# Performance work log

Measured on AMD Instinct MI355X. Metric: run time of the kernel, lower is better.

Reference implementation:

```python
import jax, jax.numpy as jnp
import numpy as np

B, T, D, F, H = 512, 48, 128, 16, 512


def setup_inputs() -> dict:
    key = jax.random.key(0)
    ks = jax.random.split(key, 7)
    return {
        "input": jax.random.normal(ks[0], (B, T, D, F), dtype=jnp.float32),
        "attn_w": jax.random.normal(ks[1], (2 * H + F * T,), dtype=jnp.float32) * 0.02,
        "attn_b": jax.random.normal(ks[2], (1,), dtype=jnp.float32) * 0.02,
        "w_ih": jax.random.normal(ks[3], (4 * H, D * F), dtype=jnp.float32) * 0.02,
        "w_hh": jax.random.normal(ks[4], (4 * H, H), dtype=jnp.float32) * 0.02,
        "b_ih": jax.random.normal(ks[5], (4 * H,), dtype=jnp.float32) * 0.02,
        "b_hh": jax.random.normal(ks[6], (4 * H,), dtype=jnp.float32) * 0.02,
    }


def reference(input, attn_w, attn_b, w_ih, w_hh, b_ih, b_hh):
    Bsz, Ts, Dn, Fn = input.shape
    Hs = w_hh.shape[1]
    # permute(0,2,3,1): [B, T, D, F] -> [B, D, F, T]
    x_perm = jnp.transpose(input, (0, 2, 3, 1))
    x_flat = x_perm.reshape(Bsz, Dn, Fn * Ts)  # [B, D, F*T]
    # encode_attn input is concat(hidden, cell, x); split the weight accordingly
    w_h, w_c, w_x = attn_w[:Hs], attn_w[Hs:2 * Hs], attn_w[2 * Hs:]
    # x contribution to attention logits is constant across steps
    e_x = x_flat @ w_x + attn_b[0]             # [B, D]
    xs = jnp.moveaxis(x_perm, 3, 0)            # [T, B, D, F] (time-major for scan)
    bias = b_ih + b_hh                         # fuse the two LSTM biases

    def step(carry, x_t):
        h, c = carry                           # [B, H] each
        e = e_x + (h @ w_h)[:, None] + (c @ w_c)[:, None]  # [B, D]
        a = jax.nn.softmax(e, axis=-1)
        x_hat = (a[:, :, None] * x_t).reshape(Bsz, Dn * Fn)  # [B, D*F]
        gates = x_hat @ w_ih.T + h @ w_hh.T + bias            # [B, 4H]
        i, f, g, o = jnp.split(gates, 4, axis=-1)  # torch LSTM gate order
        c_new = jax.nn.sigmoid(f) * c + jax.nn.sigmoid(i) * jnp.tanh(g)
        h_new = jax.nn.sigmoid(o) * jnp.tanh(c_new)
        return (h_new, c_new), h_new

    h0 = jnp.zeros((Bsz, Hs), dtype=input.dtype)
    _, hs = jax.lax.scan(step, (h0, h0), xs)   # hs: [T, B, H]
    return jnp.transpose(hs, (1, 0, 2))        # [B, T, H] == hidden_states[:, 1:]
```

## Files before the change

kernel.cpp:

```cpp
#include <hip/hip_runtime.h>

#define B_ 512
#define T_ 48
#define D_ 128
#define F_ 16
#define H_ 512

typedef float f32x4 __attribute__((ext_vector_type(4)));
typedef short s16x8 __attribute__((ext_vector_type(8)));
typedef unsigned short u16x8 __attribute__((ext_vector_type(8)));
typedef unsigned short u16x4 __attribute__((ext_vector_type(4)));
typedef unsigned long long u64;

__device__ __forceinline__ unsigned short f2bf(float x) {
  unsigned u = __float_as_uint(x);
  u += 0x7fffu + ((u >> 16) & 1u);
  return (unsigned short)(u >> 16);
}
__device__ __forceinline__ float bf2f(unsigned short h) {
  return __uint_as_float(((unsigned)h) << 16);
}
__device__ __forceinline__ float fsig(float x) {
  float e = __builtin_amdgcn_exp2f(-1.442695041f * x);
  return __builtin_amdgcn_rcpf(1.f + e);
}
__device__ __forceinline__ float ftanh(float x) {
  float e = __builtin_amdgcn_exp2f(2.885390082f * x);
  return 1.f - 2.f * __builtin_amdgcn_rcpf(1.f + e);
}

__device__ __forceinline__ void st_sys_u64(u64* p, u64 v) {
  __hip_atomic_store(p, v, __ATOMIC_RELAXED, __HIP_MEMORY_SCOPE_SYSTEM);
}
__device__ __forceinline__ u64 ld_sys_u64(const u64* p) {
  return __hip_atomic_load((u64*)p, __ATOMIC_RELAXED, __HIP_MEMORY_SCOPE_SYSTEM);
}
__device__ __forceinline__ void st_sys_u16(unsigned short* p, unsigned short v) {
  __hip_atomic_store(p, v, __ATOMIC_RELAXED, __HIP_MEMORY_SCOPE_SYSTEM);
}
__device__ __forceinline__ void st_sys_u32(unsigned* p, unsigned v) {
  __hip_atomic_store(p, v, __ATOMIC_RELAXED, __HIP_MEMORY_SCOPE_SYSTEM);
}
__device__ __forceinline__ unsigned ld_sys_u32(const unsigned* p) {
  return __hip_atomic_load((unsigned*)p, __ATOMIC_RELAXED, __HIP_MEMORY_SCOPE_SYSTEM);
}

#define AS1 __attribute__((address_space(1)))
#define AS3 __attribute__((address_space(3)))
__device__ __forceinline__ void g2lds16(const void* g, void* l) {
  __builtin_amdgcn_global_load_lds((const AS1 void*)g, (AS3 void*)l, 16, 0, 0);
}

__global__ __launch_bounds__(256) void k_prep(const float* __restrict__ wih,
                                              const float* __restrict__ whh,
                                              unsigned short* __restrict__ wih_b,
                                              unsigned short* __restrict__ whh_b) {
  long i4 = ((long)blockIdx.x * 256 + threadIdx.x) * 4;
  if (i4 < 4194304) {
    float4 v = *(const float4*)(wih + i4);
    u16x4 o = {f2bf(v.x), f2bf(v.y), f2bf(v.z), f2bf(v.w)};
    *(u16x4*)(wih_b + i4) = o;
  } else {
    long j = i4 - 4194304;
    if (j < 1048576) {
      float4 v = *(const float4*)(whh + j);
      u16x4 o = {f2bf(v.x), f2bf(v.y), f2bf(v.z), f2bf(v.w)};
      *(u16x4*)(whh_b + j) = o;
    }
  }
}

__global__ __launch_bounds__(128) void k_ex(const float* __restrict__ in,
                                            const float* __restrict__ attn_w,
                                            const float* __restrict__ attn_b,
                                            float* __restrict__ a_out) {
  __shared__ float wx[768];
  __shared__ float red[128];
  const int b = blockIdx.x, d = threadIdx.x;
  for (int i = d; i < 768; i += 128) wx[i] = attn_w[1024 + i];
  __syncthreads();
  const float* base = in + (long)b * 98304 + (long)d * 16;
  float acc = 0.f;
  for (int t = 0; t < 48; ++t) {
    const float4* p = (const float4*)(base + (long)t * 2048);
    float4 v0 = p[0], v1 = p[1], v2 = p[2], v3 = p[3];
    acc += v0.x * wx[t]       + v0.y * wx[48 + t]  + v0.z * wx[96 + t]  + v0.w * wx[144 + t];
    acc += v1.x * wx[192 + t] + v1.y * wx[240 + t] + v1.z * wx[288 + t] + v1.w * wx[336 + t];
    acc += v2.x * wx[384 + t] + v2.y * wx[432 + t] + v2.z * wx[480 + t] + v2.w * wx[528 + t];
    acc += v3.x * wx[576 + t] + v3.y * wx[624 + t] + v3.z * wx[672 + t] + v3.w * wx[720 + t];
  }
  acc += attn_b[0];
  red[d] = acc;
  __syncthreads();
  for (int s = 64; s > 0; s >>= 1) {
    if (d < s) red[d] = fmaxf(red[d], red[d + s]);
    __syncthreads();
  }
  float mx = red[0];
  __syncthreads();
  float ex = expf(acc - mx);
  red[d] = ex;
  __syncthreads();
  for (int s = 64; s > 0; s >>= 1) {
    if (d < s) red[d] += red[d + s];
    __syncthreads();
  }
  a_out[b * 128 + d] = ex / red[0];
}

__global__ __launch_bounds__(256) void k_xhat(const float* __restrict__ in,
                                              const float* __restrict__ a,
                                              unsigned short* __restrict__ xh) {
  const int mrow = blockIdx.x;
  const int t = mrow >> 9, b = mrow & 511;
  const int tid = threadIdx.x;
  const int k = tid * 8;
  const int d = k >> 4;
  const int f0 = k & 15;
  const float* src = in + (((long)(b * 48 + t) * 128 + d) * 16 + f0);
  float4 v0 = *(const float4*)src;
  float4 v1 = *(const float4*)(src + 4);
  float s = a[b * 128 + d];
  u16x8 o;
  o[0] = f2bf(v0.x * s); o[1] = f2bf(v0.y * s); o[2] = f2bf(v0.z * s); o[3] = f2bf(v0.w * s);
  o[4] = f2bf(v1.x * s); o[5] = f2bf(v1.y * s); o[6] = f2bf(v1.z * s); o[7] = f2bf(v1.w * s);
  *(u16x8*)(xh + (long)mrow * 2048 + k) = o;
}

#define G_STAGEA(ktv, s)                                                        \
  do {                                                                          \
    const long ko_ = (long)(ktv) * 64 + (long)(s) * 262144;                     \
    char* la_ = (char*)SM + ((ktv) & 1) * 32768 + (s) * 16384 + ldsw;           \
    g2lds16(Ag + ko_, la_);                                                     \
    g2lds16(Ag + ko_ + 131072, la_ + 8192);                                     \
  } while (0)

#define G_LDA4(dst, bufel, ksv, mh)                                             \
  do {                                                                          \
    const unsigned short* ab_ =                                                 \
        SM + (bufel) + aBase + (mh) * 4096 + (psw ^ ((ksv) * 32));              \
    dst[0] = *(const s16x8*)(ab_);                                              \
    dst[1] = *(const s16x8*)(ab_ + 1024);                                       \
    dst[2] = *(const s16x8*)(ab_ + 2048);                                       \
    dst[3] = *(const s16x8*)(ab_ + 3072);                                       \
  } while (0)

#define G_LDBG(dst, ktv)                                                        \
  do {                                                                          \
    const unsigned short* bp_ = Bg + (long)(ktv) * 64;                          \
    _Pragma("unroll") for (int nt_ = 0; nt_ < 4; ++nt_)                         \
        _Pragma("unroll") for (int ks_ = 0; ks_ < 2; ++ks_)                     \
            dst[nt_][ks_] = *(const s16x8*)(bp_ + nt_ * 16 * 2048 + ks_ * 32);  \
  } while (0)

#define G_MMA2(mh, Af, BC, ksv)                                                 \
  do {                                                                          \
    __builtin_amdgcn_s_setprio(1);                                              \
    _Pragma("unroll") for (int mt_ = 0; mt_ < 4; ++mt_)                         \
        _Pragma("unroll") for (int nt_ = 0; nt_ < 4; ++nt_)                     \
            acc[(mh) * 4 + mt_][nt_] = __builtin_amdgcn_mfma_f32_16x16x32_bf16( \
                Af[mt_], BC[nt_][ksv], acc[(mh) * 4 + mt_][nt_], 0, 0, 0);      \
    __builtin_amdgcn_s_setprio(0);                                              \
  } while (0)

#define G_GATE(n) asm volatile("s_waitcnt vmcnt(" #n ")" ::: "memory")

#define G_TILE(ktv, BC, BN)                                                     \
  do {                                                                          \
    const int bufel_ = ((ktv) & 1) * 16384;                                     \
    s16x8 a0[4], a1[4];                                                         \
    G_LDBG(BN, (ktv) + 1);                                                      \
    G_LDA4(a0, bufel_, 0, 0);                                                   \
    G_STAGEA((ktv) + 1, 0);                                                     \
    G_STAGEA((ktv) + 1, 1);                                                     \
    G_MMA2(0, a0, BC, 0);                                                       \
    G_LDA4(a1, bufel_, 0, 1);                                                   \
    G_MMA2(1, a1, BC, 0);                                                       \
    G_LDA4(a0, bufel_, 1, 0);                                                   \
    G_MMA2(0, a0, BC, 1);                                                       \
    G_LDA4(a1, bufel_, 1, 1);                                                   \
    G_MMA2(1, a1, BC, 1);                                                       \
    G_GATE(0);                                                                  \
    __builtin_amdgcn_s_barrier();                                               \
  } while (0)

__global__ __launch_bounds__(512, 2) void k_gemm(const unsigned short* __restrict__ A,
                                                 const unsigned short* __restrict__ Bw,
                                                 unsigned short* __restrict__ C) {
  __shared__ __align__(16) unsigned short SM[32768];
  const int tid = threadIdx.x;
  const int w = tid >> 6, lane = tid & 63;
  const int q = lane >> 4, l16 = lane & 15;
  const int wm = w >> 2, wn = w & 3;
  const int id = blockIdx.x;
  const int xcd = id & 7, j = id >> 3;
  const long m0 = ((long)xcd * 12 + (j >> 3)) * 256;
  const long n0 = (long)(j & 7) * 256;

  const int srow = w * 8 + (lane >> 3);
  const int csrc = (lane & 7) ^ (lane >> 3);
  const unsigned short* Ag = A + (m0 + srow) * 2048 + csrc * 8;
  const int ldsw = w * 1024;

  const unsigned short* Bg = Bw + (n0 + wn * 64 + l16) * 2048 + q * 8;

  const int psw = (q ^ (l16 & 7)) * 8;
  const int aBase = (wm * 128 + l16) * 64;

  f32x4 acc[8][4];
  const f32x4 zz = {0.f, 0.f, 0.f, 0.f};
#pragma unroll
  for (int i = 0; i < 8; ++i)
#pragma unroll
    for (int j2 = 0; j2 < 4; ++j2) acc[i][j2] = zz;

  s16x8 bA[4][2], bB[4][2];
  G_LDBG(bA, 0);
  G_STAGEA(0, 0);
  G_STAGEA(0, 1);
  G_GATE(0);
  __builtin_amdgcn_s_barrier();

#pragma unroll 1
  for (int kt2 = 0; kt2 < 15; ++kt2) {
    const int kt = kt2 * 2;
    G_TILE(kt, bA, bB);
    G_TILE(kt + 1, bB, bA);
  }
  G_TILE(30, bA, bB);
  {
    s16x8 a0[4], a1[4];
    G_LDA4(a0, 16384, 0, 0);
    G_MMA2(0, a0, bB, 0);
    G_LDA4(a1, 16384, 0, 1);
    G_MMA2(1, a1, bB, 0);
    G_LDA4(a0, 16384, 1, 0);
    G_MMA2(0, a0, bB, 1);
    G_LDA4(a1, 16384, 1, 1);
    G_MMA2(1, a1, bB, 1);
  }

#pragma unroll
  for (int mh = 0; mh < 2; ++mh)
#pragma unroll
    for (int mt = 0; mt < 4; ++mt)
#pragma unroll
      for (int nt = 0; nt < 4; ++nt)
#pragma unroll
        for (int r = 0; r < 4; ++r) {
          long m = m0 + wm * 128 + mh * 64 + mt * 16 + q * 4 + r;
          long n = n0 + wn * 64 + nt * 16 + l16;
          C[m * 2048 + n] = f2bf(acc[mh * 4 + mt][nt][r]);
        }
}

__global__ __launch_bounds__(256, 1) void k_rec(const unsigned short* __restrict__ gx,
                                                const unsigned short* __restrict__ whh_b,
                                                const float* __restrict__ b_ih,
                                                const float* __restrict__ b_hh,
                                                unsigned short* __restrict__ h_buf,
                                                float* __restrict__ out,
                                                unsigned int* __restrict__ bar) {
  __shared__ __align__(16) float slab[16 * 32 * 36];
  __shared__ __align__(16) unsigned short hs_own[32 * 40];
  const int tid = threadIdx.x;
  const int w = tid >> 6, lane = tid & 63;
  const int q = lane >> 4, l16 = lane & 15;
  const int bt = blockIdx.x & 15, g = blockIdx.x >> 4;
  const int b0 = bt * 32;
  const int pj = tid & 31;
  const int pr0 = (tid >> 5) * 4;
  unsigned int* slots = &bar[bt * 16];
  const int ownw = ((g >> 2) == w);
  const int ownc = g & 3;

  s16x8 wreg[32];
#pragma unroll
  for (int quad = 0; quad < 4; ++quad)
#pragma unroll
    for (int nt = 0; nt < 2; ++nt)
#pragma unroll
      for (int ci = 0; ci < 4; ++ci) {
        const unsigned short* wp =
            whh_b + (long)(quad * 512 + g * 32 + nt * 16 + l16) * 512 + (w * 4 + ci) * 32 + q * 8;
        asm volatile("global_load_dwordx4 %0, %1, off"
                     : "=v"(wreg[(quad * 2 + nt) * 4 + ci]) : "v"(wp) : "memory");
      }
  asm volatile("s_waitcnt vmcnt(0)" ::: "memory");
  __builtin_amdgcn_sched_barrier(0);

  float bias_[4];
#pragma unroll
  for (int qq = 0; qq < 4; ++qq) {
    int jj = qq * 512 + g * 32 + pj;
    bias_[qq] = b_ih[jj] + b_hh[jj];
  }
  float creg[4] = {0.f, 0.f, 0.f, 0.f};
  const f32x4 zz = {0.f, 0.f, 0.f, 0.f};

#define LD_CHUNK(slot, ci)                                                      \
  do {                                                                          \
    long o_ = hbase + (w * 4 + (ci)) * 8;                                       \
    L[slot][0] = ld_sys_u64(hb + o_);                                           \
    L[slot][1] = ld_sys_u64(hb + o_ + 1);                                       \
    L[slot][2] = ld_sys_u64(hb + o_ + 2048);                                    \
    L[slot][3] = ld_sys_u64(hb + o_ + 2049);                                    \
  } while (0)

  for (int t = 0; t < 48; ++t) {
    unsigned short gxr[4][4];
    const unsigned short* gp = gx + ((long)t * 512 + b0 + pr0) * 2048 + g * 32 + pj;
#pragma unroll
    for (int rr = 0; rr < 4; ++rr)
#pragma unroll
      for (int qq = 0; qq < 4; ++qq)
        gxr[qq][rr] = gp[rr * 2048 + qq * 512];

    if (t > 0) {
      const int need = (lane < 4) && !(ownw && lane == ownc);
      const unsigned* fp = &slots[w * 4 + (lane & 3)];
      while (1) {
        unsigned v = need ? ld_sys_u32(fp) : 0xffffffffu;
        if (__all((int)(v >= (unsigned)t))) break;
      }
      u64 L[2][4];
      const u64* hb = (const u64*)(h_buf + ((t - 1) & 1) * (512 * 512));
      const long hbase = (long)(b0 + l16) * 128 + q * 2;
      f32x4 acc[4][2][2];
#pragma unroll
      for (int a = 0; a < 4; ++a)
#pragma unroll
        for (int b = 0; b < 2; ++b)
#pragma unroll
          for (int c = 0; c < 2; ++c) acc[a][b][c] = zz;
      if (!(ownw && 0 == ownc)) LD_CHUNK(0, 0);
#pragma unroll
      for (int ci = 0; ci < 4; ++ci) {
        if (ci < 3 && !(ownw && (ci + 1) == ownc)) LD_CHUNK((ci + 1) & 1, ci + 1);
        s16x8 af0, af1;
        if (ownw && ci == ownc) {
          af0 = *(const s16x8*)&hs_own[l16 * 40 + q * 8];
          af1 = *(const s16x8*)&hs_own[(16 + l16) * 40 + q * 8];
        } else {
          union { u64 u[2]; s16x8 v; } c0, c1;
          c0.u[0] = L[ci & 1][0]; c0.u[1] = L[ci & 1][1];
          c1.u[0] = L[ci & 1][2]; c1.u[1] = L[ci & 1][3];
          af0 = c0.v; af1 = c1.v;
        }
#pragma unroll
        for (int quad = 0; quad < 4; ++quad)
#pragma unroll
          for (int nt = 0; nt < 2; ++nt) {
            acc[quad][nt][0] = __builtin_amdgcn_mfma_f32_16x16x32_bf16(
                af0, wreg[(quad * 2 + nt) * 4 + ci], acc[quad][nt][0], 0, 0, 0);
            acc[quad][nt][1] = __builtin_amdgcn_mfma_f32_16x16x32_bf16(
                af1, wreg[(quad * 2 + nt) * 4 + ci], acc[quad][nt][1], 0, 0, 0);
          }
      }
#pragma unroll
      for (int quad = 0; quad < 4; ++quad)
#pragma unroll
        for (int nt = 0; nt < 2; ++nt)
#pragma unroll
          for (int mh = 0; mh < 2; ++mh)
            *(f32x4*)&slab[((w * 4 + quad) * 32 + nt * 16 + l16) * 36 + mh * 16 + q * 4] =
                acc[quad][nt][mh];
    }
    __syncthreads();

    float hval[4];
    {
      f32x4 gs[4];
      if (t > 0) {
#pragma unroll
        for (int qq = 0; qq < 4; ++qq) {
          f32x4 s0 = *(const f32x4*)&slab[((0 * 4 + qq) * 32 + pj) * 36 + pr0];
          f32x4 s1 = *(const f32x4*)&slab[((1 * 4 + qq) * 32 + pj) * 36 + pr0];
          f32x4 s2 = *(const f32x4*)&slab[((2 * 4 + qq) * 32 + pj) * 36 + pr0];
          f32x4 s3 = *(const f32x4*)&slab[((3 * 4 + qq) * 32 + pj) * 36 + pr0];
          gs[qq] = (s0 + s1) + (s2 + s3);
        }
      } else {
#pragma unroll
        for (int qq = 0; qq < 4; ++qq) gs[qq] = zz;
      }
#pragma unroll
      for (int rr = 0; rr < 4; ++rr) {
        float g0 = gs[0][rr] + bias_[0] + bf2f(gxr[0][rr]);
        float g1 = gs[1][rr] + bias_[1] + bf2f(gxr[1][rr]);
        float g2 = gs[2][rr] + bias_[2] + bf2f(gxr[2][rr]);
        float g3 = gs[3][rr] + bias_[3] + bf2f(gxr[3][rr]);
        float is = fsig(g0);
        float fs = fsig(g1);
        float gt = ftanh(g2);
        float os = fsig(g3);
        creg[rr] = fs * creg[rr] + is * gt;
        hval[rr] = os * ftanh(creg[rr]);
      }
    }
#pragma unroll
    for (int rr = 0; rr < 4; ++rr) {
      unsigned short hb16 = f2bf(hval[rr]);
      hs_own[(pr0 + rr) * 40 + pj] = hb16;
      st_sys_u16(&h_buf[(t & 1) * (512 * 512) + (b0 + pr0 + rr) * 512 + g * 32 + pj], hb16);
    }
    __syncthreads();
    if (t < 47 && tid == 0)
      st_sys_u32(&slots[g], (unsigned)(t + 1));
#pragma unroll
    for (int rr = 0; rr < 4; ++rr)
      __builtin_nontemporal_store(
          hval[rr], &out[(long)(b0 + pr0 + rr) * (T_ * H_) + (long)t * H_ + g * 32 + pj]);
  }
#undef LD_CHUNK
}

extern "C" void kernel_launch(void* const* d_in, const int* in_sizes, int n_in,
                              void* d_out, int out_size, void* d_ws, size_t ws_size,
                              hipStream_t stream) {
  const float* input  = (const float*)d_in[0];
  const float* attn_w = (const float*)d_in[1];
  const float* attn_b = (const float*)d_in[2];
  const float* w_ih   = (const float*)d_in[3];
  const float* w_hh   = (const float*)d_in[4];
  const float* b_ih   = (const float*)d_in[5];
  const float* b_hh   = (const float*)d_in[6];
  float* out = (float*)d_out;

  char* ws = (char*)d_ws;
  unsigned int* bar     = (unsigned int*)ws;
  float* a_ws           = (float*)(ws + 1024);
  unsigned short* h_buf = (unsigned short*)(ws + 263168);
  unsigned short* whh_b = (unsigned short*)(ws + 1311744);
  unsigned short* wih_b = (unsigned short*)(ws + 3408896);
  unsigned short* x_hat = (unsigned short*)(ws + 11797504);
  unsigned short* gxws  = (unsigned short*)(ws + 112460800);

  (void)hipMemsetAsync(d_ws, 0, 1024, stream);
  hipLaunchKernelGGL(k_prep, dim3(5120), dim3(256), 0, stream, w_ih, w_hh, wih_b, whh_b);
  hipLaunchKernelGGL(k_ex, dim3(512), dim3(128), 0, stream, input, attn_w, attn_b, a_ws);
  hipLaunchKernelGGL(k_xhat, dim3(24576), dim3(256), 0, stream, input, a_ws, x_hat);
  hipLaunchKernelGGL(k_gemm, dim3(768), dim3(512), 0, stream, x_hat, wih_b, gxws);
  hipLaunchKernelGGL(k_rec, dim3(256), dim3(256), 0, stream, gxws, whh_b, b_ih, b_hh, h_buf, out, bar);
}
```

Baseline: 852.1 us.

## Stage GEMM B tiles through LDS and split k_ex time loop across two halves

```diff
diff --git a/kernel.cpp b/kernel.cpp
--- a/kernel.cpp
+++ b/kernel.cpp
@@ -70,18 +70,20 @@
   }
 }
 
-__global__ __launch_bounds__(128) void k_ex(const float* __restrict__ in,
+__global__ __launch_bounds__(256) void k_ex(const float* __restrict__ in,
                                             const float* __restrict__ attn_w,
                                             const float* __restrict__ attn_b,
                                             float* __restrict__ a_out) {
   __shared__ float wx[768];
+  __shared__ float red2[256];
   __shared__ float red[128];
-  const int b = blockIdx.x, d = threadIdx.x;
-  for (int i = d; i < 768; i += 128) wx[i] = attn_w[1024 + i];
+  const int b = blockIdx.x, tid = threadIdx.x;
+  const int d = tid & 127, half = tid >> 7;
+  for (int i = tid; i < 768; i += 256) wx[i] = attn_w[1024 + i];
   __syncthreads();
   const float* base = in + (long)b * 98304 + (long)d * 16;
   float acc = 0.f;
-  for (int t = 0; t < 48; ++t) {
+  for (int t = half * 24; t < half * 24 + 24; ++t) {
     const float4* p = (const float4*)(base + (long)t * 2048);
     float4 v0 = p[0], v1 = p[1], v2 = p[2], v3 = p[3];
     acc += v0.x * wx[t]       + v0.y * wx[48 + t]  + v0.z * wx[96 + t]  + v0.w * wx[144 + t];
@@ -89,23 +91,31 @@
     acc += v2.x * wx[384 + t] + v2.y * wx[432 + t] + v2.z * wx[480 + t] + v2.w * wx[528 + t];
     acc += v3.x * wx[576 + t] + v3.y * wx[624 + t] + v3.z * wx[672 + t] + v3.w * wx[720 + t];
   }
-  acc += attn_b[0];
-  red[d] = acc;
+  red2[tid] = acc;
+  __syncthreads();
+  float a2 = 0.f;
+  if (tid < 128) {
+    a2 = red2[tid] + red2[tid + 128] + attn_b[0];
+    red[tid] = a2;
+  }
   __syncthreads();
   for (int s = 64; s > 0; s >>= 1) {
-    if (d < s) red[d] = fmaxf(red[d], red[d + s]);
+    if (tid < s) red[tid] = fmaxf(red[tid], red[tid + s]);
     __syncthreads();
   }
   float mx = red[0];
   __syncthreads();
-  float ex = expf(acc - mx);
-  red[d] = ex;
+  float ex = 0.f;
+  if (tid < 128) {
+    ex = expf(a2 - mx);
+    red[tid] = ex;
+  }
   __syncthreads();
   for (int s = 64; s > 0; s >>= 1) {
-    if (d < s) red[d] += red[d + s];
+    if (tid < s) red[tid] += red[tid + s];
     __syncthreads();
   }
-  a_out[b * 128 + d] = ex / red[0];
+  if (tid < 128) a_out[b * 128 + d] = ex / red[0];
 }
 
 __global__ __launch_bounds__(256) void k_xhat(const float* __restrict__ in,
@@ -127,12 +137,15 @@
   *(u16x8*)(xh + (long)mrow * 2048 + k) = o;
 }
 
-#define G_STAGEA(ktv, s)                                                        \
+
+#define G_STAGE(ktv, s)                                                         \
   do {                                                                          \
     const long ko_ = (long)(ktv) * 64 + (long)(s) * 262144;                     \
     char* la_ = (char*)SM + ((ktv) & 1) * 32768 + (s) * 16384 + ldsw;           \
     g2lds16(Ag + ko_, la_);                                                     \
     g2lds16(Ag + ko_ + 131072, la_ + 8192);                                     \
+    g2lds16(Bg + ko_, la_ + 65536);                                             \
+    g2lds16(Bg + ko_ + 131072, la_ + 73728);                                    \
   } while (0)
 
 #define G_LDA4(dst, bufel, ksv, mh)                                             \
@@ -145,49 +158,31 @@
     dst[3] = *(const s16x8*)(ab_ + 3072);                                       \
   } while (0)
 
-#define G_LDBG(dst, ktv)                                                        \
+#define G_LDB4(dst, bufel, ksv)                                                 \
   do {                                                                          \
-    const unsigned short* bp_ = Bg + (long)(ktv) * 64;                          \
-    _Pragma("unroll") for (int nt_ = 0; nt_ < 4; ++nt_)                         \
-        _Pragma("unroll") for (int ks_ = 0; ks_ < 2; ++ks_)                     \
-            dst[nt_][ks_] = *(const s16x8*)(bp_ + nt_ * 16 * 2048 + ks_ * 32);  \
+    const unsigned short* bb_ = SM + (bufel) + bBase + (psw ^ ((ksv) * 32));    \
+    dst[0] = *(const s16x8*)(bb_);                                              \
+    dst[1] = *(const s16x8*)(bb_ + 1024);                                       \
+    dst[2] = *(const s16x8*)(bb_ + 2048);                                       \
+    dst[3] = *(const s16x8*)(bb_ + 3072);                                       \
   } while (0)
 
-#define G_MMA2(mh, Af, BC, ksv)                                                 \
+#define G_MMA2(mh, Af, Bf)                                                      \
   do {                                                                          \
     __builtin_amdgcn_s_setprio(1);                                              \
     _Pragma("unroll") for (int mt_ = 0; mt_ < 4; ++mt_)                         \
         _Pragma("unroll") for (int nt_ = 0; nt_ < 4; ++nt_)                     \
             acc[(mh) * 4 + mt_][nt_] = __builtin_amdgcn_mfma_f32_16x16x32_bf16( \
-                Af[mt_], BC[nt_][ksv], acc[(mh) * 4 + mt_][nt_], 0, 0, 0);      \
+                Af[mt_], Bf[nt_], acc[(mh) * 4 + mt_][nt_], 0, 0, 0);           \
     __builtin_amdgcn_s_setprio(0);                                              \
   } while (0)
 
 #define G_GATE(n) asm volatile("s_waitcnt vmcnt(" #n ")" ::: "memory")
-
-#define G_TILE(ktv, BC, BN)                                                     \
-  do {                                                                          \
-    const int bufel_ = ((ktv) & 1) * 16384;                                     \
-    s16x8 a0[4], a1[4];                                                         \
-    G_LDBG(BN, (ktv) + 1);                                                      \
-    G_LDA4(a0, bufel_, 0, 0);                                                   \
-    G_STAGEA((ktv) + 1, 0);                                                     \
-    G_STAGEA((ktv) + 1, 1);                                                     \
-    G_MMA2(0, a0, BC, 0);                                                       \
-    G_LDA4(a1, bufel_, 0, 1);                                                   \
-    G_MMA2(1, a1, BC, 0);                                                       \
-    G_LDA4(a0, bufel_, 1, 0);                                                   \
-    G_MMA2(0, a0, BC, 1);                                                       \
-    G_LDA4(a1, bufel_, 1, 1);                                                   \
-    G_MMA2(1, a1, BC, 1);                                                       \
-    G_GATE(0);                                                                  \
-    __builtin_amdgcn_s_barrier();                                               \
-  } while (0)
 
 __global__ __launch_bounds__(512, 2) void k_gemm(const unsigned short* __restrict__ A,
                                                  const unsigned short* __restrict__ Bw,
                                                  unsigned short* __restrict__ C) {
-  __shared__ __align__(16) unsigned short SM[32768];
+  __shared__ __align__(16) unsigned short SM[65536];
   const int tid = threadIdx.x;
   const int w = tid >> 6, lane = tid & 63;
   const int q = lane >> 4, l16 = lane & 15;
@@ -200,12 +195,12 @@
   const int srow = w * 8 + (lane >> 3);
   const int csrc = (lane & 7) ^ (lane >> 3);
   const unsigned short* Ag = A + (m0 + srow) * 2048 + csrc * 8;
+  const unsigned short* Bg = Bw + (n0 + srow) * 2048 + csrc * 8;
   const int ldsw = w * 1024;
-
-  const unsigned short* Bg = Bw + (n0 + wn * 64 + l16) * 2048 + q * 8;
 
   const int psw = (q ^ (l16 & 7)) * 8;
   const int aBase = (wm * 128 + l16) * 64;
+  const int bBase = 32768 + (wn * 64 + l16) * 64;
 
   f32x4 acc[8][4];
   const f32x4 zz = {0.f, 0.f, 0.f, 0.f};
@@ -214,30 +209,42 @@
 #pragma unroll
     for (int j2 = 0; j2 < 4; ++j2) acc[i][j2] = zz;
 
-  s16x8 bA[4][2], bB[4][2];
-  G_LDBG(bA, 0);
-  G_STAGEA(0, 0);
-  G_STAGEA(0, 1);
+  G_STAGE(0, 0);
+  G_STAGE(0, 1);
   G_GATE(0);
   __builtin_amdgcn_s_barrier();
 
 #pragma unroll 1
-  for (int kt2 = 0; kt2 < 15; ++kt2) {
-    const int kt = kt2 * 2;
-    G_TILE(kt, bA, bB);
-    G_TILE(kt + 1, bB, bA);
-  }
-  G_TILE(30, bA, bB);
+  for (int kt = 0; kt < 31; ++kt) {
+    const int bufel = (kt & 1) * 16384;
+    s16x8 b0[4], b1[4], a00[4], a01[4], a10[4], a11[4];
+    G_LDB4(b0, bufel, 0);
+    G_LDA4(a00, bufel, 0, 0);
+    G_STAGE(kt + 1, 0);
+    G_LDA4(a01, bufel, 0, 1);
+    G_STAGE(kt + 1, 1);
+    G_MMA2(0, a00, b0);
+    G_LDB4(b1, bufel, 1);
+    G_LDA4(a10, bufel, 1, 0);
+    G_MMA2(1, a01, b0);
+    G_LDA4(a11, bufel, 1, 1);
+    G_MMA2(0, a10, b1);
+    G_MMA2(1, a11, b1);
+    G_GATE(0);
+    __builtin_amdgcn_s_barrier();
+  }
   {
-    s16x8 a0[4], a1[4];
-    G_LDA4(a0, 16384, 0, 0);
-    G_MMA2(0, a0, bB, 0);
-    G_LDA4(a1, 16384, 0, 1);
-    G_MMA2(1, a1, bB, 0);
-    G_LDA4(a0, 16384, 1, 0);
-    G_MMA2(0, a0, bB, 1);
-    G_LDA4(a1, 16384, 1, 1);
-    G_MMA2(1, a1, bB, 1);
+    s16x8 b0[4], b1[4], a00[4], a01[4], a10[4], a11[4];
+    G_LDB4(b0, 16384, 0);
+    G_LDA4(a00, 16384, 0, 0);
+    G_LDA4(a01, 16384, 0, 1);
+    G_MMA2(0, a00, b0);
+    G_LDB4(b1, 16384, 1);
+    G_LDA4(a10, 16384, 1, 0);
+    G_MMA2(1, a01, b0);
+    G_LDA4(a11, 16384, 1, 1);
+    G_MMA2(0, a10, b1);
+    G_MMA2(1, a11, b1);
   }
 
 #pragma unroll
@@ -438,7 +445,7 @@
 
   (void)hipMemsetAsync(d_ws, 0, 1024, stream);
   hipLaunchKernelGGL(k_prep, dim3(5120), dim3(256), 0, stream, w_ih, w_hh, wih_b, whh_b);
-  hipLaunchKernelGGL(k_ex, dim3(512), dim3(128), 0, stream, input, attn_w, attn_b, a_ws);
+  hipLaunchKernelGGL(k_ex, dim3(512), dim3(256), 0, stream, input, attn_w, attn_b, a_ws);
   hipLaunchKernelGGL(k_xhat, dim3(24576), dim3(256), 0, stream, input, a_ws, x_hat);
   hipLaunchKernelGGL(k_gemm, dim3(768), dim3(512), 0, stream, x_hat, wih_b, gxws);
   hipLaunchKernelGGL(k_rec, dim3(256), dim3(256), 0, stream, gxws, whh_b, b_ih, b_hh, h_buf, out, bar);
```

Result: faster. 741.0 us (-13.0%).
